# Optimization experiments

Measured on AMD Instinct MI355X. Metric: run time of the kernel, lower is better.

Reference implementation:

```python
import jax, jax.numpy as jnp
import numpy as np

NUM_HEADS = 16


def setup_inputs() -> dict:
    key = jax.random.key(0)
    ks = jax.random.split(key, 8)
    B, L, Hd = 2, 2048, 1024
    s = 0.02
    return {
        "x": jax.random.normal(ks[0], (B, L, Hd), jnp.float32),
        "y": jax.random.normal(ks[1], (B, L, Hd), jnp.float32),
        "mask": jnp.zeros((B, L), jnp.bool_),  # True = padding (masked out)
        "Wq_w": jax.random.normal(ks[2], (Hd, Hd), jnp.float32) * s,
        "Wq_b": jnp.zeros((Hd,), jnp.float32),
        "Wkv_w": jax.random.normal(ks[3], (Hd, 2 * Hd), jnp.float32) * s,
        "Wkv_b": jnp.zeros((2 * Hd,), jnp.float32),
        "proj_w": jax.random.normal(ks[4], (Hd, Hd), jnp.float32) * s,
        "proj_b": jnp.zeros((Hd,), jnp.float32),
    }


def reference(x, y, mask, Wq_w, Wq_b, Wkv_w, Wkv_b, proj_w, proj_b):
    B, L, Hd = x.shape
    H = NUM_HEADS
    D = Hd // H
    scale = 1.0 / np.sqrt(D)

    # projections (torch Linear: stored here already as (in, out))
    q = (x @ Wq_w + Wq_b).reshape(B, L, H, D).transpose(0, 2, 1, 3)   # bhld
    kv = (y @ Wkv_w + Wkv_b).reshape(B, L, 2, H, D)
    k = kv[:, :, 0].transpose(0, 2, 1, 3)                             # bhkd
    v = kv[:, :, 1].transpose(0, 2, 1, 3)                             # bhkd

    attn = jnp.einsum("bhld,bhkd->bhlk", q, k) * scale

    # combined padding (over keys) + causal mask; True = masked
    causal = jnp.triu(jnp.ones((L, L), jnp.bool_), 1)                 # (L, L)
    combined = mask[:, None, None, :] | causal[None, None]            # (B,1,L,L)
    attn = jnp.where(combined, -jnp.inf, attn)

    p = jax.nn.softmax(attn, axis=-1)
    out = jnp.einsum("bhlk,bhkd->bhld", p, v)
    out = out.transpose(0, 2, 1, 3).reshape(B, L, Hd)
    return out @ proj_w + proj_b
```

## Files before the change

kernel.cpp:

```cpp
#include <hip/hip_runtime.h>
#include <stdint.h>

#define B_  2
#define L_  2048
#define HD_ 1024
#define H_  16
#define D_  64

typedef unsigned short u16;
typedef __attribute__((ext_vector_type(8))) short bf16x8;
typedef __attribute__((ext_vector_type(4))) float f32x4;

#define MFMA16(a, b, c) __builtin_amdgcn_mfma_f32_16x16x32_bf16((a), (b), (c), 0, 0, 0)

__device__ __forceinline__ void gload16(const void* g, void* l) {
  __builtin_amdgcn_global_load_lds((const __attribute__((address_space(1))) void*)g,
                                   (__attribute__((address_space(3))) void*)l, 16, 0, 0);
}

__device__ __forceinline__ u16 f2bf(float f) {
  union { float f; uint32_t u; } c; c.f = f;
  uint32_t u = c.u + 0x7FFFu + ((c.u >> 16) & 1u);
  return (u16)(u >> 16);
}

__device__ __forceinline__ uint32_t cvt_pk_bf16(float lo, float hi) {
  uint32_t r;
  asm("v_cvt_pk_bf16_f32 %0, %1, %2" : "=v"(r) : "v"(lo), "v"(hi));
  return r;
}

__global__ void cast2_k(const float* __restrict__ x, const float* __restrict__ y,
                        u16* __restrict__ xb, u16* __restrict__ yb) {
  int bid = blockIdx.x;
  const float* in = bid < 2048 ? x : y;
  u16* out = bid < 2048 ? xb : yb;
  int i = ((bid & 2047) * 256 + threadIdx.x) * 8;
  float4 a = *(const float4*)(in + i);
  float4 b = *(const float4*)(in + i + 4);
  bf16x8 r;
  r[0] = (short)f2bf(a.x); r[1] = (short)f2bf(a.y); r[2] = (short)f2bf(a.z); r[3] = (short)f2bf(a.w);
  r[4] = (short)f2bf(b.x); r[5] = (short)f2bf(b.y); r[6] = (short)f2bf(b.z); r[7] = (short)f2bf(b.w);
  *(bf16x8*)(out + i) = r;
}

__global__ void wtrans_k(const float* __restrict__ Wq, const float* __restrict__ Wkv,
                         const float* __restrict__ Wp,
                         u16* __restrict__ Wqt, u16* __restrict__ Wkvt, u16* __restrict__ Wpt) {
  int z = blockIdx.z;
  const float* src = z == 0 ? Wq : (z == 1 ? Wkv : Wp);
  u16* dst = z == 0 ? Wqt : (z == 1 ? Wkvt : Wpt);
  int Nfull = (z == 1) ? 2048 : 1024;
  int nb = blockIdx.x * 32;
  if (nb >= Nfull) return;
  __shared__ float tile[32][33];
  int t = threadIdx.x;
  int tc = t & 31, tr = t >> 5;
  int kb = blockIdx.y * 32;
#pragma unroll
  for (int i = 0; i < 4; i++)
    tile[tr + i * 8][tc] = src[(size_t)(kb + tr + i * 8) * Nfull + nb + tc];
  __syncthreads();
#pragma unroll
  for (int i = 0; i < 4; i++) {
    int nl = tr + i * 8;
    dst[(size_t)(nb + nl) * 1024 + kb + tc] = f2bf(tile[tc][nl]);
  }
}

__device__ __forceinline__ void gemm_body(
    char* sA, char* sB,
    const u16* __restrict__ A, const u16* __restrict__ Bt,
    const float* __restrict__ bias, void* __restrict__ outp,
    int N, int epi, int bm, int bn)
{
  int t = threadIdx.x;
  int lane = t & 63, w = t >> 6;
  int g = lane >> 4, l15 = lane & 15;
  int wr = w >> 1, wc = w & 1;

  f32x4 zero = {0.f, 0.f, 0.f, 0.f};
  f32x4 acc[4][4];
#pragma unroll
  for (int mi = 0; mi < 4; mi++)
#pragma unroll
    for (int ni = 0; ni < 4; ni++) acc[mi][ni] = zero;

#define GSTAGE(bufi, k0s) do {                                                          \
    _Pragma("unroll")                                                                   \
    for (int it = 0; it < 4; it++) {                                                    \
      int c = it * 256 + t;                          \
      int r = c >> 3, sp = c & 7;                                                       \
      int off = (sp ^ (r & 7)) << 4;               \
      gload16((const char*)(A + (size_t)(bm + r) * 1024 + (k0s)) + off,                 \
              sA + (bufi) * 16384 + c * 16);                                            \
      gload16((const char*)(Bt + (size_t)(bn + r) * 1024 + (k0s)) + off,                \
              sB + (bufi) * 16384 + c * 16);                                            \
    } } while (0)

  GSTAGE(0, 0);
  int buf = 0;
#pragma unroll 1
  for (int kt = 0; kt < 16; kt++) {
    __builtin_amdgcn_sched_barrier(0);
    __builtin_amdgcn_s_barrier();
    if (kt < 15) {
      GSTAGE(buf ^ 1, (kt + 1) << 6);
      asm volatile("s_waitcnt vmcnt(8)" ::: "memory");
    } else {
      asm volatile("s_waitcnt vmcnt(0)" ::: "memory");
    }
    __builtin_amdgcn_s_barrier();
    __builtin_amdgcn_sched_barrier(0);

    const char* cA = sA + buf * 16384;
    const char* cB = sB + buf * 16384;
#pragma unroll
    for (int kc = 0; kc < 2; kc++) {
      bf16x8 af[4], bfr[4];
#pragma unroll
      for (int mi = 0; mi < 4; mi++) {
        int r = wr * 64 + mi * 16 + l15;
        af[mi] = *(const bf16x8*)(cA + r * 128 + (((kc * 4 + g) ^ (r & 7)) << 4));
      }
#pragma unroll
      for (int ni = 0; ni < 4; ni++) {
        int r = wc * 64 + ni * 16 + l15;
        bfr[ni] = *(const bf16x8*)(cB + r * 128 + (((kc * 4 + g) ^ (r & 7)) << 4));
      }
#pragma unroll
      for (int mi = 0; mi < 4; mi++)
#pragma unroll
        for (int ni = 0; ni < 4; ni++)
          acc[mi][ni] = MFMA16(af[mi], bfr[ni], acc[mi][ni]);
    }
    buf ^= 1;
  }
#undef GSTAGE

  float bv[4];
#pragma unroll
  for (int ni = 0; ni < 4; ni++) bv[ni] = bias[bn + wc * 64 + ni * 16 + l15];

  if (epi == 2) {
    float* fo = (float*)outp;
#pragma unroll
    for (int mi = 0; mi < 4; mi++)
#pragma unroll
      for (int ni = 0; ni < 4; ni++) {
        int n = bn + wc * 64 + ni * 16 + l15;
#pragma unroll
        for (int r = 0; r < 4; r++) {
          int m = bm + wr * 64 + mi * 16 + g * 4 + r;
          fo[(size_t)m * N + n] = acc[mi][ni][r] + bv[ni];
        }
      }
  } else {
    u16* ob = (u16*)outp;
#pragma unroll
    for (int mi = 0; mi < 4; mi++)
#pragma unroll
      for (int ni = 0; ni < 4; ni++) {
        int n = bn + wc * 64 + ni * 16 + l15;
        int kv = n >> 10;
        int hh = (n >> 6) & 15;
        int dd = n & 63;
        int m0 = bm + wr * 64 + mi * 16 + g * 4;
        int bb = m0 >> 11, lq0 = m0 & 2047;
        if (epi == 1 && kv == 1) {
          ushort4 pk;
          pk.x = f2bf(acc[mi][ni][0] + bv[ni]);
          pk.y = f2bf(acc[mi][ni][1] + bv[ni]);
          pk.z = f2bf(acc[mi][ni][2] + bv[ni]);
          pk.w = f2bf(acc[mi][ni][3] + bv[ni]);
          size_t idx = (size_t)(B_ * H_ * L_ * D_) +
                       (((size_t)(bb * H_ + hh) * D_ + dd) * L_ + lq0);
          *(ushort4*)(ob + idx) = pk;
        } else {
#pragma unroll
          for (int r = 0; r < 4; r++) {
            size_t idx = (((size_t)(bb * H_ + hh) * L_ + lq0 + r) * D_) + dd;
            ob[idx] = f2bf(acc[mi][ni][r] + bv[ni]);
          }
        }
      }
  }
}

__global__ __launch_bounds__(256) void qkv_k(
    const u16* __restrict__ xb, const u16* __restrict__ yb,
    const u16* __restrict__ Wqt, const u16* __restrict__ Wkvt,
    const float* __restrict__ Wq_b, const float* __restrict__ Wkv_b,
    u16* __restrict__ Qout, u16* __restrict__ KVout)
{
  __shared__ char sA[2 * 16384];
  __shared__ char sB[2 * 16384];
  int bx = blockIdx.x, bm = blockIdx.y * 128;
  if (bx < 8)
    gemm_body(sA, sB, xb, Wqt, Wq_b, (void*)Qout, 1024, 0, bm, bx * 128);
  else
    gemm_body(sA, sB, yb, Wkvt, Wkv_b, (void*)KVout, 2048, 1, bm, (bx - 8) * 128);
}

__global__ __launch_bounds__(256) void gemm_k(
    const u16* __restrict__ A, const u16* __restrict__ Bt,
    const float* __restrict__ bias, void* __restrict__ outp, int N)
{
  __shared__ char sA[2 * 16384];
  __shared__ char sB[2 * 16384];
  gemm_body(sA, sB, A, Bt, bias, outp, N, 2, blockIdx.y * 128, blockIdx.x * 128);
}

__global__ __launch_bounds__(512, 2) void attn_k(
    const u16* __restrict__ Qb, const u16* __restrict__ Kb, const u16* __restrict__ Vt,
    const unsigned char* __restrict__ pad, u16* __restrict__ Ob)
{
  __shared__ char sK[2][8192];
  __shared__ char sV[2][8192];
  __shared__ char sP[8][2048];
  int t = threadIdx.x, lane = t & 63, w = t >> 6, g = lane >> 4, l15 = lane & 15;
  int x = blockIdx.x, h = blockIdx.y, b = blockIdx.z, bh = b * H_ + h;
  int qb = b ? x : 15 - x;

  const u16* Kbh = Kb + (size_t)bh * L_ * D_;
  const u16* Vbh = Vt + (size_t)bh * D_ * L_;
  const unsigned char* pdb = pad + b * L_;
  const float SCL = 0.125f * 1.44269504089f;
  int psw = l15 & 7;

  int srr = t >> 3, ssp = t & 7;
  int sso = (ssp ^ (srr & 7)) << 4;
#define STAGE(bufi, kt0s) do {                                                        \
    gload16((const char*)(Kbh + (size_t)((kt0s) + srr) * D_) + sso, sK[bufi] + t * 16); \
    gload16((const char*)(Vbh + (size_t)srr * L_ + (kt0s)) + sso, sV[bufi] + t * 16);   \
  } while (0)

  int qw0 = qb * 128 + w * 16;
  int bound = qw0 + 15;
  int nkt = 2 * qb + 2;

  const u16* qp = Qb + ((size_t)bh * L_ + qw0 + l15) * D_ + g * 8;
  bf16x8 qf0 = *(const bf16x8*)qp;
  bf16x8 qf1 = *(const bf16x8*)(qp + 32);

  f32x4 zero = {0.f, 0.f, 0.f, 0.f};
  f32x4 oacc[4];
#pragma unroll
  for (int db = 0; db < 4; db++) oacc[db] = zero;
  float mrun = -1e30f, lrun = 0.f;

  STAGE(0, 0);
  int buf = 0;

#pragma unroll 1
  for (int kt = 0; kt < nkt; kt++) {
    int kt0 = kt << 6;
    __builtin_amdgcn_sched_barrier(0);
    __builtin_amdgcn_s_barrier();
    if (kt + 1 < nkt) {
      STAGE(buf ^ 1, (kt + 1) << 6);
      asm volatile("s_waitcnt vmcnt(2)" ::: "memory");
    } else {
      asm volatile("s_waitcnt vmcnt(0)" ::: "memory");
    }
    __builtin_amdgcn_s_barrier();
    __builtin_amdgcn_sched_barrier(0);

    if (kt0 <= bound) {
      float sc[4][4];
#pragma unroll
      for (int s = 0; s < 4; s++) {
        int kb = kt0 + s * 16;
        bool live = (kb <= bound);
        f32x4 st = zero;
        uint32_t pb = 0;
        if (live) {
          int R = s * 16 + l15, sw = l15 & 7;
          bf16x8 kf0 = *(const bf16x8*)(sK[buf] + R * 128 + ((g ^ sw) << 4));
          bf16x8 kf1 = *(const bf16x8*)(sK[buf] + R * 128 + (((4 + g) ^ sw) << 4));
          st = MFMA16(kf0, qf0, st);
          st = MFMA16(kf1, qf1, st);
          pb = *(const uint32_t*)(pdb + kb + 4 * g);
        }
        bool needm = !live || (kb + 15 > qw0) || (__ballot(pb != 0) != 0);
        if (needm) {
#pragma unroll
          for (int r = 0; r < 4; r++) {
            int key = kb + 4 * g + r;
            bool pm = (pb >> (8 * r)) & 0xffu;
            bool msk = !live || pm || (key > qw0 + l15);
            sc[s][r] = msk ? -1e30f : st[r] * SCL;
          }
        } else {
#pragma unroll
          for (int r = 0; r < 4; r++) sc[s][r] = st[r] * SCL;
        }
      }

      float m0 = fmaxf(fmaxf(sc[0][0], sc[0][1]), fmaxf(sc[0][2], sc[0][3]));
      float m1 = fmaxf(fmaxf(sc[1][0], sc[1][1]), fmaxf(sc[1][2], sc[1][3]));
      float m2 = fmaxf(fmaxf(sc[2][0], sc[2][1]), fmaxf(sc[2][2], sc[2][3]));
      float m3 = fmaxf(fmaxf(sc[3][0], sc[3][1]), fmaxf(sc[3][2], sc[3][3]));
      float mt = fmaxf(fmaxf(m0, m1), fmaxf(m2, m3));
      mt = fmaxf(mt, __shfl_xor(mt, 16));
      mt = fmaxf(mt, __shfl_xor(mt, 32));
      float mnew = fmaxf(mrun, mt);
      float al = __builtin_amdgcn_exp2f(mrun - mnew);
      mrun = mnew;
      float rs = 0.f;
      char* pwb = sP[w] + l15 * 128 + (g & 1) * 8;
#pragma unroll
      for (int s = 0; s < 4; s++) {
        float p0 = __builtin_amdgcn_exp2f(sc[s][0] - mnew);
        float p1 = __builtin_amdgcn_exp2f(sc[s][1] - mnew);
        float p2 = __builtin_amdgcn_exp2f(sc[s][2] - mnew);
        float p3 = __builtin_amdgcn_exp2f(sc[s][3] - mnew);
        rs += (p0 + p1) + (p2 + p3);
        uint32_t w0 = cvt_pk_bf16(p0, p1), w1 = cvt_pk_bf16(p2, p3);
        char* dst = pwb + (((2 * s + (g >> 1)) ^ psw) << 4);
        *(uint32_t*)dst = w0;
        *(uint32_t*)(dst + 4) = w1;
      }
      rs += __shfl_xor(rs, 16);
      rs += __shfl_xor(rs, 32);
      lrun = lrun * al + rs;
#pragma unroll
      for (int db = 0; db < 4; db++)
#pragma unroll
        for (int r = 0; r < 4; r++) oacc[db][r] *= al;

#pragma unroll
      for (int kc = 0; kc < 2; kc++) {
        if (kt0 + 32 * kc <= bound) {
          bf16x8 pf = *(const bf16x8*)(sP[w] + l15 * 128 + (((4 * kc + g) ^ psw) << 4));
#pragma unroll
          for (int db = 0; db < 4; db++) {
            int dR = db * 16 + l15;
            bf16x8 vf = *(const bf16x8*)(sV[buf] + dR * 128 +
                                         (((4 * kc + g) ^ (dR & 7)) << 4));
            oacc[db] = MFMA16(vf, pf, oacc[db]);
          }
        }
      }
    }
    buf ^= 1;
  }

  float rl = 1.0f / lrun;
  int q = qw0 + l15;
  u16* op = Ob + ((size_t)b * L_ + q) * HD_ + h * D_ + g * 4;
#pragma unroll
  for (int db = 0; db < 4; db++) {
    ushort4 pk;
    pk.x = f2bf(oacc[db][0] * rl);
    pk.y = f2bf(oacc[db][1] * rl);
    pk.z = f2bf(oacc[db][2] * rl);
    pk.w = f2bf(oacc[db][3] * rl);
    *(ushort4*)(op + db * 16) = pk;
  }
#undef STAGE
}

extern "C" void kernel_launch(void* const* d_in, const int* in_sizes, int n_in,
                              void* d_out, int out_size, void* d_ws, size_t ws_size,
                              hipStream_t stream) {
  const float* x      = (const float*)d_in[0];
  const float* y      = (const float*)d_in[1];
  const unsigned char* mask = (const unsigned char*)d_in[2];
  const float* Wq_w   = (const float*)d_in[3];
  const float* Wq_b   = (const float*)d_in[4];
  const float* Wkv_w  = (const float*)d_in[5];
  const float* Wkv_b  = (const float*)d_in[6];
  const float* proj_w = (const float*)d_in[7];
  const float* proj_b = (const float*)d_in[8];

  char* ws = (char*)d_ws;
  u16* xb   = (u16*)(ws);
  u16* yb   = (u16*)(ws + (size_t)(8  << 20));
  u16* Wqt  = (u16*)(ws + (size_t)(16 << 20));
  u16* Wkvt = (u16*)(ws + (size_t)(18 << 20));
  u16* Wpt  = (u16*)(ws + (size_t)(22 << 20));
  u16* Qb   = (u16*)(ws + (size_t)(24 << 20));
  u16* Kb   = (u16*)(ws + (size_t)(32 << 20));
  u16* Vtb  = (u16*)(ws + (size_t)(40 << 20));
  u16* Ob   = xb;

  hipLaunchKernelGGL(cast2_k, dim3(4096), dim3(256), 0, stream, x, y, xb, yb);
  hipLaunchKernelGGL(wtrans_k, dim3(64, 32, 3), dim3(256), 0, stream,
                     Wq_w, Wkv_w, proj_w, Wqt, Wkvt, Wpt);
  hipLaunchKernelGGL(qkv_k, dim3(24, 32), dim3(256), 0, stream,
                     xb, yb, Wqt, Wkvt, Wq_b, Wkv_b, Qb, Kb);
  hipLaunchKernelGGL(attn_k, dim3(16, H_, B_), dim3(512), 0, stream, Qb, Kb, Vtb, mask, Ob);
  hipLaunchKernelGGL(gemm_k, dim3(8, 32), dim3(256), 0, stream, Ob, Wpt, proj_b, d_out, 1024);
}
```

Baseline: 136.3 us.

## Split heavy causal query blocks across two workgroups and merge partial results

The eight heaviest causal query blocks per head (query rows 1024 and up) now have their key range split into two halves, each run by its own workgroup. Each half writes a normalized bf16 partial output plus its running max and sum, and a new merge kernel combines them with log-sum-exp weights. This evens out work per workgroup and raises the grid from 512 to 768 blocks to cut tail imbalance. The cost is an extra kernel launch, extra global traffic for the partials, and an added bf16 rounding step on the merged output.

```diff
diff --git a/kernel.cpp b/kernel.cpp
--- a/kernel.cpp
+++ b/kernel.cpp
@@ -22,6 +22,11 @@
   union { float f; uint32_t u; } c; c.f = f;
   uint32_t u = c.u + 0x7FFFu + ((c.u >> 16) & 1u);
   return (u16)(u >> 16);
+}
+
+__device__ __forceinline__ float bf2f(u16 v) {
+  union { uint32_t u; float f; } c; c.u = (uint32_t)v << 16;
+  return c.f;
 }
 
 __device__ __forceinline__ uint32_t cvt_pk_bf16(float lo, float hi) {
@@ -213,14 +218,29 @@
 
 __global__ __launch_bounds__(512, 2) void attn_k(
     const u16* __restrict__ Qb, const u16* __restrict__ Kb, const u16* __restrict__ Vt,
-    const unsigned char* __restrict__ pad, u16* __restrict__ Ob)
+    const unsigned char* __restrict__ pad, u16* __restrict__ Ob,
+    u16* __restrict__ Opart, float* __restrict__ mlbuf)
 {
   __shared__ char sK[2][8192];
   __shared__ char sV[2][8192];
   __shared__ char sP[8][2048];
   int t = threadIdx.x, lane = t & 63, w = t >> 6, g = lane >> 4, l15 = lane & 15;
   int x = blockIdx.x, h = blockIdx.y, b = blockIdx.z, bh = b * H_ + h;
-  int qb = b ? x : 15 - x;
+
+  int qb, kt_lo, kt_hi, part;
+  bool split = (x < 16);
+  if (split) {
+    qb = 15 - (x >> 1);
+    part = x & 1;
+    int half = qb + 1;
+    kt_lo = part ? half : 0;
+    kt_hi = part ? 2 * qb + 2 : half;
+  } else {
+    qb = 23 - x;
+    part = 0;
+    kt_lo = 0;
+    kt_hi = 2 * qb + 2;
+  }
 
   const u16* Kbh = Kb + (size_t)bh * L_ * D_;
   const u16* Vbh = Vt + (size_t)bh * D_ * L_;
@@ -237,8 +257,6 @@
 
   int qw0 = qb * 128 + w * 16;
   int bound = qw0 + 15;
-  int nkt = 2 * qb + 2;
-
   const u16* qp = Qb + ((size_t)bh * L_ + qw0 + l15) * D_ + g * 8;
   bf16x8 qf0 = *(const bf16x8*)qp;
   bf16x8 qf1 = *(const bf16x8*)(qp + 32);
@@ -249,15 +267,15 @@
   for (int db = 0; db < 4; db++) oacc[db] = zero;
   float mrun = -1e30f, lrun = 0.f;
 
-  STAGE(0, 0);
+  STAGE(0, kt_lo << 6);
   int buf = 0;
 
 #pragma unroll 1
-  for (int kt = 0; kt < nkt; kt++) {
+  for (int kt = kt_lo; kt < kt_hi; kt++) {
     int kt0 = kt << 6;
     __builtin_amdgcn_sched_barrier(0);
     __builtin_amdgcn_s_barrier();
-    if (kt + 1 < nkt) {
+    if (kt + 1 < kt_hi) {
       STAGE(buf ^ 1, (kt + 1) << 6);
       asm volatile("s_waitcnt vmcnt(2)" ::: "memory");
     } else {
@@ -348,17 +366,59 @@
 
   float rl = 1.0f / lrun;
   int q = qw0 + l15;
-  u16* op = Ob + ((size_t)b * L_ + q) * HD_ + h * D_ + g * 4;
-#pragma unroll
-  for (int db = 0; db < 4; db++) {
-    ushort4 pk;
-    pk.x = f2bf(oacc[db][0] * rl);
-    pk.y = f2bf(oacc[db][1] * rl);
-    pk.z = f2bf(oacc[db][2] * rl);
-    pk.w = f2bf(oacc[db][3] * rl);
-    *(ushort4*)(op + db * 16) = pk;
+  if (!split) {
+    u16* op = Ob + ((size_t)b * L_ + q) * HD_ + h * D_ + g * 4;
+#pragma unroll
+    for (int db = 0; db < 4; db++) {
+      ushort4 pk;
+      pk.x = f2bf(oacc[db][0] * rl);
+      pk.y = f2bf(oacc[db][1] * rl);
+      pk.z = f2bf(oacc[db][2] * rl);
+      pk.w = f2bf(oacc[db][3] * rl);
+      *(ushort4*)(op + db * 16) = pk;
+    }
+  } else {
+    size_t prow = (size_t)part * 32768 + (size_t)bh * 1024 + (q - 1024);
+    u16* op = Opart + prow * 64 + g * 4;
+#pragma unroll
+    for (int db = 0; db < 4; db++) {
+      ushort4 pk;
+      pk.x = f2bf(oacc[db][0] * rl);
+      pk.y = f2bf(oacc[db][1] * rl);
+      pk.z = f2bf(oacc[db][2] * rl);
+      pk.w = f2bf(oacc[db][3] * rl);
+      *(ushort4*)(op + db * 16) = pk;
+    }
+    if (g == 0) {
+      mlbuf[prow * 2]     = mrun;
+      mlbuf[prow * 2 + 1] = lrun;
+    }
   }
 #undef STAGE
+}
+
+__global__ __launch_bounds__(256) void merge_k(
+    const u16* __restrict__ Op, const float* __restrict__ ml, u16* __restrict__ Ob)
+{
+  int tid = blockIdx.x * 256 + threadIdx.x;
+  int d0 = (tid & 7) * 8;
+  int row = tid >> 3;
+  int qrel = row & 1023, bh = row >> 10;
+  int b = bh >> 4, h = bh & 15;
+  float m0 = ml[(size_t)row * 2],            l0 = ml[(size_t)row * 2 + 1];
+  float m1 = ml[((size_t)32768 + row) * 2],  l1 = ml[((size_t)32768 + row) * 2 + 1];
+  float M = fmaxf(m0, m1);
+  float w0 = l0 * __builtin_amdgcn_exp2f(m0 - M);
+  float w1 = l1 * __builtin_amdgcn_exp2f(m1 - M);
+  float rw = 1.0f / (w0 + w1);
+  w0 *= rw; w1 *= rw;
+  bf16x8 a = *(const bf16x8*)(Op + (size_t)row * 64 + d0);
+  bf16x8 c = *(const bf16x8*)(Op + ((size_t)32768 + row) * 64 + d0);
+  bf16x8 o;
+#pragma unroll
+  for (int j = 0; j < 8; j++)
+    o[j] = (short)f2bf(w0 * bf2f((u16)a[j]) + w1 * bf2f((u16)c[j]));
+  *(bf16x8*)(Ob + ((size_t)b * L_ + 1024 + qrel) * HD_ + h * D_ + d0) = o;
 }
 
 extern "C" void kernel_launch(void* const* d_in, const int* in_sizes, int n_in,
@@ -384,12 +444,16 @@
   u16* Kb   = (u16*)(ws + (size_t)(32 << 20));
   u16* Vtb  = (u16*)(ws + (size_t)(40 << 20));
   u16* Ob   = xb;
+  u16* Opart  = yb;
+  float* mlbuf = (float*)Wqt;
 
   hipLaunchKernelGGL(cast2_k, dim3(4096), dim3(256), 0, stream, x, y, xb, yb);
   hipLaunchKernelGGL(wtrans_k, dim3(64, 32, 3), dim3(256), 0, stream,
                      Wq_w, Wkv_w, proj_w, Wqt, Wkvt, Wpt);
   hipLaunchKernelGGL(qkv_k, dim3(24, 32), dim3(256), 0, stream,
                      xb, yb, Wqt, Wkvt, Wq_b, Wkv_b, Qb, Kb);
-  hipLaunchKernelGGL(attn_k, dim3(16, H_, B_), dim3(512), 0, stream, Qb, Kb, Vtb, mask, Ob);
+  hipLaunchKernelGGL(attn_k, dim3(24, H_, B_), dim3(512), 0, stream,
+                     Qb, Kb, Vtb, mask, Ob, Opart, mlbuf);
+  hipLaunchKernelGGL(merge_k, dim3(1024), dim3(256), 0, stream, Opart, mlbuf, Ob);
   hipLaunchKernelGGL(gemm_k, dim3(8, 32), dim3(256), 0, stream, Ob, Wpt, proj_b, d_out, 1024);
 }
```

Result: slower. 148.6 us (+9.0%).
